# Kernel tuning notes

Hardware: AMD Instinct MI355X
Metric: run time of the kernel (lower is better)

The kernel has to match this reference:

```python
import jax, jax.numpy as jnp
import numpy as np

B, S, H = 4, 2048, 1024

def setup_inputs() -> dict:
    key = jax.random.key(0)
    k = jax.random.split(key, 5)
    scale = 1.0 / np.sqrt(H)
    return {
        "hidden": jax.random.normal(k[0], (B, S, H), dtype=jnp.float32),
        "mask": jnp.zeros((B, 1, S, S), dtype=jnp.float32),
        "R": jax.random.normal(k[1], (S, S), dtype=jnp.float32),
        "G_w": jax.random.normal(k[2], (H, H), dtype=jnp.float32) * scale,
        "G_b": jnp.zeros((H,), dtype=jnp.float32),
        "F_w": jax.random.normal(k[3], (H, H), dtype=jnp.float32) * scale,
        "F_b": jnp.zeros((H,), dtype=jnp.float32),
    }

def reference(hidden, mask, R, G_w, G_b, F_w, F_b):
    # scores: [B, S, S] = learned random bias + additive attention mask
    scores = R + mask[:, 0]
    probs = jax.nn.softmax(scores, axis=-1)  # dropout is identity in eval mode
    values = jnp.einsum('bsh,oh->bso', hidden, G_w) + G_b  # G_linear
    out = jnp.einsum('bqk,bkh->bqh', probs, values)
    out = jnp.einsum('bsh,oh->bso', out, F_w) + F_b  # final_linear
    return out
```

## Files before the change

### kernel.cpp

```cpp
#include <hip/hip_runtime.h>
#include <hip/hip_bf16.h>

typedef __bf16 bf16x8 __attribute__((ext_vector_type(8)));
typedef __bf16 bf16x4 __attribute__((ext_vector_type(4)));
typedef float  f32x16 __attribute__((ext_vector_type(16)));

#define GPTR(p) ((__attribute__((address_space(1))) void*)(p))
#define LPTR(p) ((__attribute__((address_space(3))) void*)(p))

__global__ __launch_bounds__(256) void pre_kernel(
    const float* __restrict__ Fw, __bf16* __restrict__ f_bf,
    const float* __restrict__ Gw, __bf16* __restrict__ gt_bf,
    const float* __restrict__ Gb, const float* __restrict__ Fb,
    float* __restrict__ b2, int H) {
    __shared__ float tile[64][65];
    const int blk = blockIdx.x;
    const int t = threadIdx.x;

    if (blk < 512) {
        long i = ((long)blk * 256 + t) * 8;
        float4 a = *reinterpret_cast<const float4*>(Fw + i);
        float4 c = *reinterpret_cast<const float4*>(Fw + i + 4);
        bf16x8 o;
        o[0] = (__bf16)a.x; o[1] = (__bf16)a.y; o[2] = (__bf16)a.z; o[3] = (__bf16)a.w;
        o[4] = (__bf16)c.x; o[5] = (__bf16)c.y; o[6] = (__bf16)c.z; o[7] = (__bf16)c.w;
        *reinterpret_cast<bf16x8*>(f_bf + i) = o;
    } else if (blk < 768) {
        const int id = blk - 512;
        const int bx = (id & 15) * 64;
        const int by = (id >> 4) * 64;
        const int tr = t >> 4;
        const int tc = (t & 15) * 4;
#pragma unroll
        for (int i = 0; i < 4; i++) {
            float4 v = *reinterpret_cast<const float4*>(&Gw[(size_t)(by + tr + i * 16) * H + bx + tc]);
            tile[tr + i * 16][tc + 0] = v.x;
            tile[tr + i * 16][tc + 1] = v.y;
            tile[tr + i * 16][tc + 2] = v.z;
            tile[tr + i * 16][tc + 3] = v.w;
        }
        __syncthreads();
        const int wr = t >> 2;
        const int wc = (t & 3) * 16;
        bf16x8 o0, o1;
#pragma unroll
        for (int j = 0; j < 8; j++) o0[j] = (__bf16)tile[wc + j][wr];
#pragma unroll
        for (int j = 0; j < 8; j++) o1[j] = (__bf16)tile[wc + 8 + j][wr];
        *reinterpret_cast<bf16x8*>(&gt_bf[(size_t)(bx + wr) * H + by + wc]) = o0;
        *reinterpret_cast<bf16x8*>(&gt_bf[(size_t)(bx + wr) * H + by + wc + 8]) = o1;
    } else {
        const int o = blk - 768;
        float s = 0.f;
        for (int h = t; h < H; h += 256) s += Fw[(size_t)o * H + h] * Gb[h];
#pragma unroll
        for (int off = 32; off > 0; off >>= 1) s += __shfl_xor(s, off);
        __shared__ float ss[4];
        if ((t & 63) == 0) ss[t >> 6] = s;
        __syncthreads();
        if (t == 0) b2[o] = ss[0] + ss[1] + ss[2] + ss[3] + Fb[o];
    }
}

__global__ __launch_bounds__(256) void mid_kernel(
    const __bf16* __restrict__ f_bf, const __bf16* __restrict__ gt_bf,
    __bf16* __restrict__ Wm,
    const float* __restrict__ hidden, __bf16* __restrict__ xt,
    const float* __restrict__ R, const float* __restrict__ mask,
    __bf16* __restrict__ P, int H, int S) {
    const int blk = blockIdx.x;
    const int t = threadIdx.x;

    if (blk < 256) {
        __shared__ __bf16 As[64 * 64];
        __shared__ __bf16 Bs[64 * 64];
        const int lane = t & 63;
        const int wave = t >> 6;
        const int lane31 = lane & 31;
        const int hi = lane >> 5;
        const int wm = (wave >> 1) * 32;
        const int wn = (wave & 1) * 32;
        const int bm = (blk >> 4) * 64;
        const int bn = (blk & 15) * 64;

        const int rsub = lane >> 3;
        const int csub = lane & 7;
        const int lchunk = csub ^ rsub;
        const __bf16* ga0 = f_bf + (size_t)(bm + wave * 16 + rsub) * H + lchunk * 8;
        const __bf16* gb0 = gt_bf + (size_t)(bn + wave * 16 + rsub) * H + lchunk * 8;

        f32x16 acc = (f32x16)(0.f);
        for (int kt = 0; kt < H; kt += 64) {
            __syncthreads();
#pragma unroll
            for (int c = 0; c < 2; c++)
                __builtin_amdgcn_global_load_lds(GPTR(ga0 + (size_t)(c * 8) * H + kt),
                                                 LPTR(&As[(wave * 16 + c * 8) * 64]), 16, 0, 0);
#pragma unroll
            for (int c = 0; c < 2; c++)
                __builtin_amdgcn_global_load_lds(GPTR(gb0 + (size_t)(c * 8) * H + kt),
                                                 LPTR(&Bs[(wave * 16 + c * 8) * 64]), 16, 0, 0);
            __syncthreads();
#pragma unroll
            for (int s = 0; s < 4; s++) {
                const int ra = wm + lane31;
                const int rb = wn + lane31;
                bf16x8 af = *reinterpret_cast<const bf16x8*>(
                    &As[ra * 64 + (((2 * s + hi) ^ (ra & 7)) << 3)]);
                bf16x8 bfr = *reinterpret_cast<const bf16x8*>(
                    &Bs[rb * 64 + (((2 * s + hi) ^ (rb & 7)) << 3)]);
                acc = __builtin_amdgcn_mfma_f32_32x32x16_bf16(af, bfr, acc, 0, 0, 0);
            }
        }
        const int cm = bm + wm;
        const int cn = bn + wn + lane31;
#pragma unroll
        for (int rq = 0; rq < 4; rq++) {
            const int rbase = rq * 8 + 4 * hi;
#pragma unroll
            for (int rr = 0; rr < 4; rr++)
                Wm[(size_t)(cm + rbase + rr) * H + cn] = (__bf16)acc[rq * 4 + rr];
        }
    } else if (blk < 2304) {
        __shared__ float tile[64][65];
        const int id = blk - 256;
        const int b = id >> 9;
        const int tid = id & 511;
        const int by = (tid >> 4) * 64;
        const int bx = (tid & 15) * 64;
        const float* x = hidden + (size_t)b * S * H;
        __bf16* y = xt + (size_t)b * H * S;
        const int tr = t >> 4;
        const int tc = (t & 15) * 4;
#pragma unroll
        for (int i = 0; i < 4; i++) {
            float4 v = *reinterpret_cast<const float4*>(&x[(size_t)(by + tr + i * 16) * H + bx + tc]);
            tile[tr + i * 16][tc + 0] = v.x;
            tile[tr + i * 16][tc + 1] = v.y;
            tile[tr + i * 16][tc + 2] = v.z;
            tile[tr + i * 16][tc + 3] = v.w;
        }
        __syncthreads();
        const int wr = t >> 2;
        const int wc = (t & 3) * 16;
        bf16x8 o0, o1;
#pragma unroll
        for (int j = 0; j < 8; j++) o0[j] = (__bf16)tile[wc + j][wr];
#pragma unroll
        for (int j = 0; j < 8; j++) o1[j] = (__bf16)tile[wc + 8 + j][wr];
        *reinterpret_cast<bf16x8*>(&y[(size_t)(bx + wr) * S + by + wc]) = o0;
        *reinterpret_cast<bf16x8*>(&y[(size_t)(bx + wr) * S + by + wc + 8]) = o1;
    } else {
        const int id = blk - 2304;
        const int b = id >> 11;
        const int q = id & 2047;
        const int lane = t & 63, wave = t >> 6;
        const float* rrow = R + (size_t)q * S;
        const float* mrow = mask + ((size_t)b * S + q) * (size_t)S;
        __bf16* prow = P + ((size_t)b * S + q) * (size_t)S;

        float v[8];
#pragma unroll
        for (int i = 0; i < 2; i++) {
            float4 r4 = *reinterpret_cast<const float4*>(rrow + t * 8 + i * 4);
            float4 m4 = *reinterpret_cast<const float4*>(mrow + t * 8 + i * 4);
            v[i * 4 + 0] = r4.x + m4.x;
            v[i * 4 + 1] = r4.y + m4.y;
            v[i * 4 + 2] = r4.z + m4.z;
            v[i * 4 + 3] = r4.w + m4.w;
        }
        float mx = v[0];
#pragma unroll
        for (int i = 1; i < 8; i++) mx = fmaxf(mx, v[i]);
#pragma unroll
        for (int off = 32; off > 0; off >>= 1) mx = fmaxf(mx, __shfl_xor(mx, off));
        __shared__ float smax[4], ssum[4];
        if (lane == 0) smax[wave] = mx;
        __syncthreads();
        mx = fmaxf(fmaxf(smax[0], smax[1]), fmaxf(smax[2], smax[3]));
        float sum = 0.f;
#pragma unroll
        for (int i = 0; i < 8; i++) { v[i] = __expf(v[i] - mx); sum += v[i]; }
#pragma unroll
        for (int off = 32; off > 0; off >>= 1) sum += __shfl_xor(sum, off);
        if (lane == 0) ssum[wave] = sum;
        __syncthreads();
        sum = ssum[0] + ssum[1] + ssum[2] + ssum[3];
        const float inv = 1.0f / sum;
        bf16x8 o;
#pragma unroll
        for (int i = 0; i < 8; i++) o[i] = (__bf16)(v[i] * inv);
        *reinterpret_cast<bf16x8*>(prow + t * 8) = o;
    }
}

template <bool CFLOAT, bool BIAS, int SWZMODE>
__global__ __launch_bounds__(256) void gemm_nt_kernel(
    const __bf16* __restrict__ A, const __bf16* __restrict__ B,
    const float* __restrict__ bias, void* __restrict__ Cv,
    int K, int lda, int ldb, int ldc,
    long strideA, long strideB, long strideC) {
    const int t = threadIdx.x;
    const int lane = t & 63;
    const int wave = t >> 6;
    const int lane31 = lane & 31;
    const int hi = lane >> 5;
    const int wm = (wave >> 1) * 64;
    const int wn = (wave & 1) * 64;
    int bm, bn, bz;
    if constexpr (SWZMODE == 1) {
        const int id = blockIdx.x;
        const int xcd = id & 7;
        const int slot = id >> 3;
        bz = xcd >> 1;
        bm = ((xcd & 1) * 8 + (slot >> 3)) * 128;
        bn = (slot & 7) * 128;
    } else {
        const int id = blockIdx.x;
        const int xcd = id & 7;
        const int slot = id >> 3;
        bz = 0;
        bm = (xcd * 8 + (slot >> 3)) * 128;
        bn = (slot & 7) * 128;
    }

    A += (size_t)bz * strideA;
    B += (size_t)bz * strideB;

    __shared__ __bf16 smem[32768];

    const int rsub = lane >> 3;
    const int csub = lane & 7;
    const int lchunk = csub ^ rsub;
    const __bf16* ga0 = A + (size_t)(bm + wave * 32 + rsub) * lda + lchunk * 8;
    const __bf16* gb0 = B + (size_t)(bn + wave * 32 + rsub) * ldb + lchunk * 8;

    auto stage = [&](int p, int kt) {
        __bf16* As_ = smem + p * 16384;
        __bf16* Bs_ = smem + p * 16384 + 8192;
#pragma unroll
        for (int c = 0; c < 4; c++)
            __builtin_amdgcn_global_load_lds(GPTR(ga0 + (size_t)(c * 8) * lda + kt),
                                             LPTR(&As_[(wave * 32 + c * 8) * 64]), 16, 0, 0);
#pragma unroll
        for (int c = 0; c < 4; c++)
            __builtin_amdgcn_global_load_lds(GPTR(gb0 + (size_t)(c * 8) * ldb + kt),
                                             LPTR(&Bs_[(wave * 32 + c * 8) * 64]), 16, 0, 0);
    };

    f32x16 acc[2][2];
#pragma unroll
    for (int i = 0; i < 2; i++)
#pragma unroll
        for (int j = 0; j < 2; j++) acc[i][j] = (f32x16)(0.f);

    stage(0, 0);
    __syncthreads();
    int p = 0;
    for (int kt = 0; kt < K; kt += 64) {
        if (kt + 64 < K) stage(p ^ 1, kt + 64);
        const __bf16* As = smem + p * 16384;
        const __bf16* Bs = smem + p * 16384 + 8192;
#pragma unroll
        for (int s = 0; s < 4; s++) {
            bf16x8 af[2], bfr[2];
#pragma unroll
            for (int mi = 0; mi < 2; mi++) {
                const int r = wm + mi * 32 + lane31;
                af[mi] = *reinterpret_cast<const bf16x8*>(
                    &As[r * 64 + (((2 * s + hi) ^ (r & 7)) << 3)]);
            }
#pragma unroll
            for (int ni = 0; ni < 2; ni++) {
                const int r = wn + ni * 32 + lane31;
                bfr[ni] = *reinterpret_cast<const bf16x8*>(
                    &Bs[r * 64 + (((2 * s + hi) ^ (r & 7)) << 3)]);
            }
#pragma unroll
            for (int mi = 0; mi < 2; mi++)
#pragma unroll
                for (int ni = 0; ni < 2; ni++)
                    acc[mi][ni] = __builtin_amdgcn_mfma_f32_32x32x16_bf16(af[mi], bfr[ni], acc[mi][ni], 0, 0, 0);
        }
        __syncthreads();
        p ^= 1;
    }

    __bf16* Cb = (__bf16*)Cv + (size_t)bz * strideC;
    float* Cf = (float*)Cv + (size_t)bz * strideC;
#pragma unroll
    for (int mi = 0; mi < 2; mi++)
#pragma unroll
        for (int ni = 0; ni < 2; ni++) {
            const int cm = bm + wm + mi * 32;
            const int cn = bn + wn + ni * 32 + lane31;
            const float bv = BIAS ? bias[cn] : 0.0f;
#pragma unroll
            for (int rq = 0; rq < 4; rq++) {
                const int rbase = rq * 8 + 4 * hi;
                if constexpr (CFLOAT) {
#pragma unroll
                    for (int rr = 0; rr < 4; rr++)
                        Cf[(size_t)(cm + rbase + rr) * ldc + cn] = acc[mi][ni][rq * 4 + rr] + bv;
                } else {
#pragma unroll
                    for (int rr = 0; rr < 4; rr++)
                        Cb[(size_t)(cm + rbase + rr) * ldc + cn] = (__bf16)(acc[mi][ni][rq * 4 + rr] + bv);
                }
            }
        }
}

extern "C" void kernel_launch(void* const* d_in, const int* in_sizes, int n_in,
                              void* d_out, int out_size, void* d_ws, size_t ws_size,
                              hipStream_t stream) {
    const float* hidden = (const float*)d_in[0];
    const float* mask   = (const float*)d_in[1];
    const float* R      = (const float*)d_in[2];
    const float* G_w    = (const float*)d_in[3];
    const float* G_b    = (const float*)d_in[4];
    const float* F_w    = (const float*)d_in[5];
    const float* F_b    = (const float*)d_in[6];
    float* out = (float*)d_out;

    constexpr int B = 4, S = 2048, H = 1024;
    char* ws = (char*)d_ws;
    __bf16* xt    = (__bf16*)(ws);
    __bf16* t1    = (__bf16*)(ws + (16ll << 20));
    __bf16* probs = (__bf16*)(ws + (32ll << 20));
    __bf16* f_bf  = (__bf16*)(ws + (64ll << 20));
    __bf16* gt_bf = (__bf16*)(ws + (66ll << 20));
    __bf16* Wm    = (__bf16*)(ws + (68ll << 20));
    float*  b2    = (float*)(ws + (70ll << 20));

    pre_kernel<<<1792, 256, 0, stream>>>(F_w, f_bf, G_w, gt_bf, G_b, F_b, b2, H);

    mid_kernel<<<10496, 256, 0, stream>>>(f_bf, gt_bf, Wm, hidden, xt,
                                          R, mask, probs, H, S);

    gemm_nt_kernel<false, false, 1><<<512, 256, 0, stream>>>(
        probs, xt, nullptr, t1, S, S, S, H,
        (long)S * S, (long)H * S, (long)S * H);

    gemm_nt_kernel<true, true, 2><<<512, 256, 0, stream>>>(
        t1, Wm, b2, out, H, H, H, H, 0, 0, 0);
}
```

Baseline: 222.7 us.

## Use 512-thread 256x128 GEMM with triple-buffered staged pipeline and wave-per-row softmax

Replaces the 128x128 double-buffered GEMM with a 512-thread, 256x128-tile kernel. It triple-buffers LDS, interleaves global-to-LDS prefetch between MFMA phases, and uses barriers, explicit waitcnt and setprio to overlap loads with compute. The softmax is changed to one wave per row so the block-level shared-memory reductions and syncthreads disappear. Mid-kernel shared memory is merged into a union to reduce its LDS footprint. The manual waitcnt and barrier scheduling is fragile and relies on the batch index being derived from bm, which only holds for the fixed shapes.

```diff
diff --git a/kernel.cpp b/kernel.cpp
--- a/kernel.cpp
+++ b/kernel.cpp
@@ -62,18 +62,24 @@
     }
 }
 
+union MidSmem {
+    struct { __bf16 a[64 * 64]; __bf16 b[64 * 64]; } g;
+    float tile[64][65];
+};
+
 __global__ __launch_bounds__(256) void mid_kernel(
     const __bf16* __restrict__ f_bf, const __bf16* __restrict__ gt_bf,
     __bf16* __restrict__ Wm,
     const float* __restrict__ hidden, __bf16* __restrict__ xt,
     const float* __restrict__ R, const float* __restrict__ mask,
     __bf16* __restrict__ P, int H, int S) {
+    __shared__ __align__(16) MidSmem sm;
     const int blk = blockIdx.x;
     const int t = threadIdx.x;
 
     if (blk < 256) {
-        __shared__ __bf16 As[64 * 64];
-        __shared__ __bf16 Bs[64 * 64];
+        __bf16* As = sm.g.a;
+        __bf16* Bs = sm.g.b;
         const int lane = t & 63;
         const int wave = t >> 6;
         const int lane31 = lane & 31;
@@ -122,7 +128,6 @@
                 Wm[(size_t)(cm + rbase + rr) * H + cn] = (__bf16)acc[rq * 4 + rr];
         }
     } else if (blk < 2304) {
-        __shared__ float tile[64][65];
         const int id = blk - 256;
         const int b = id >> 9;
         const int tid = id & 511;
@@ -135,35 +140,36 @@
 #pragma unroll
         for (int i = 0; i < 4; i++) {
             float4 v = *reinterpret_cast<const float4*>(&x[(size_t)(by + tr + i * 16) * H + bx + tc]);
-            tile[tr + i * 16][tc + 0] = v.x;
-            tile[tr + i * 16][tc + 1] = v.y;
-            tile[tr + i * 16][tc + 2] = v.z;
-            tile[tr + i * 16][tc + 3] = v.w;
+            sm.tile[tr + i * 16][tc + 0] = v.x;
+            sm.tile[tr + i * 16][tc + 1] = v.y;
+            sm.tile[tr + i * 16][tc + 2] = v.z;
+            sm.tile[tr + i * 16][tc + 3] = v.w;
         }
         __syncthreads();
         const int wr = t >> 2;
         const int wc = (t & 3) * 16;
         bf16x8 o0, o1;
 #pragma unroll
-        for (int j = 0; j < 8; j++) o0[j] = (__bf16)tile[wc + j][wr];
-#pragma unroll
-        for (int j = 0; j < 8; j++) o1[j] = (__bf16)tile[wc + 8 + j][wr];
+        for (int j = 0; j < 8; j++) o0[j] = (__bf16)sm.tile[wc + j][wr];
+#pragma unroll
+        for (int j = 0; j < 8; j++) o1[j] = (__bf16)sm.tile[wc + 8 + j][wr];
         *reinterpret_cast<bf16x8*>(&y[(size_t)(bx + wr) * S + by + wc]) = o0;
         *reinterpret_cast<bf16x8*>(&y[(size_t)(bx + wr) * S + by + wc + 8]) = o1;
     } else {
         const int id = blk - 2304;
-        const int b = id >> 11;
-        const int q = id & 2047;
         const int lane = t & 63, wave = t >> 6;
+        const int row = id * 4 + wave;
+        const int b = row >> 11;
+        const int q = row & 2047;
         const float* rrow = R + (size_t)q * S;
         const float* mrow = mask + ((size_t)b * S + q) * (size_t)S;
         __bf16* prow = P + ((size_t)b * S + q) * (size_t)S;
 
-        float v[8];
-#pragma unroll
-        for (int i = 0; i < 2; i++) {
-            float4 r4 = *reinterpret_cast<const float4*>(rrow + t * 8 + i * 4);
-            float4 m4 = *reinterpret_cast<const float4*>(mrow + t * 8 + i * 4);
+        float v[32];
+#pragma unroll
+        for (int i = 0; i < 8; i++) {
+            float4 r4 = *reinterpret_cast<const float4*>(rrow + i * 256 + lane * 4);
+            float4 m4 = *reinterpret_cast<const float4*>(mrow + i * 256 + lane * 4);
             v[i * 4 + 0] = r4.x + m4.x;
             v[i * 4 + 1] = r4.y + m4.y;
             v[i * 4 + 2] = r4.z + m4.z;
@@ -171,35 +177,30 @@
         }
         float mx = v[0];
 #pragma unroll
-        for (int i = 1; i < 8; i++) mx = fmaxf(mx, v[i]);
+        for (int i = 1; i < 32; i++) mx = fmaxf(mx, v[i]);
 #pragma unroll
         for (int off = 32; off > 0; off >>= 1) mx = fmaxf(mx, __shfl_xor(mx, off));
-        __shared__ float smax[4], ssum[4];
-        if (lane == 0) smax[wave] = mx;
-        __syncthreads();
-        mx = fmaxf(fmaxf(smax[0], smax[1]), fmaxf(smax[2], smax[3]));
         float sum = 0.f;
 #pragma unroll
-        for (int i = 0; i < 8; i++) { v[i] = __expf(v[i] - mx); sum += v[i]; }
+        for (int i = 0; i < 32; i++) { v[i] = __expf(v[i] - mx); sum += v[i]; }
 #pragma unroll
         for (int off = 32; off > 0; off >>= 1) sum += __shfl_xor(sum, off);
-        if (lane == 0) ssum[wave] = sum;
-        __syncthreads();
-        sum = ssum[0] + ssum[1] + ssum[2] + ssum[3];
         const float inv = 1.0f / sum;
-        bf16x8 o;
-#pragma unroll
-        for (int i = 0; i < 8; i++) o[i] = (__bf16)(v[i] * inv);
-        *reinterpret_cast<bf16x8*>(prow + t * 8) = o;
+#pragma unroll
+        for (int i = 0; i < 8; i++) {
+            bf16x4 o;
+#pragma unroll
+            for (int j = 0; j < 4; j++) o[j] = (__bf16)(v[i * 4 + j] * inv);
+            *reinterpret_cast<bf16x4*>(prow + i * 256 + lane * 4) = o;
+        }
     }
 }
 
-template <bool CFLOAT, bool BIAS, int SWZMODE>
-__global__ __launch_bounds__(256) void gemm_nt_kernel(
+template <bool CFLOAT, bool BIAS>
+__global__ __launch_bounds__(512, 2) void gemm8_nt(
     const __bf16* __restrict__ A, const __bf16* __restrict__ B,
     const float* __restrict__ bias, void* __restrict__ Cv,
-    int K, int lda, int ldb, int ldc,
-    long strideA, long strideB, long strideC) {
+    int K, int lda, int ldb, int ldc, long strideB) {
     const int t = threadIdx.x;
     const int lane = t & 63;
     const int wave = t >> 6;
@@ -207,46 +208,30 @@
     const int hi = lane >> 5;
     const int wm = (wave >> 1) * 64;
     const int wn = (wave & 1) * 64;
-    int bm, bn, bz;
-    if constexpr (SWZMODE == 1) {
-        const int id = blockIdx.x;
-        const int xcd = id & 7;
-        const int slot = id >> 3;
-        bz = xcd >> 1;
-        bm = ((xcd & 1) * 8 + (slot >> 3)) * 128;
-        bn = (slot & 7) * 128;
-    } else {
-        const int id = blockIdx.x;
-        const int xcd = id & 7;
-        const int slot = id >> 3;
-        bz = 0;
-        bm = (xcd * 8 + (slot >> 3)) * 128;
-        bn = (slot & 7) * 128;
-    }
-
-    A += (size_t)bz * strideA;
-    B += (size_t)bz * strideB;
-
-    __shared__ __bf16 smem[32768];
+
+    const int id = blockIdx.x;
+    const int xcd = id & 7;
+    const int slot = id >> 3;
+    const int bm = (xcd * 4 + (slot >> 3)) * 256;
+    const int bn = (slot & 7) * 128;
+    B += (size_t)(bm >> 11) * strideB;
+
+    __shared__ __align__(16) __bf16 smem[3 * 24576];
 
     const int rsub = lane >> 3;
     const int csub = lane & 7;
     const int lchunk = csub ^ rsub;
     const __bf16* ga0 = A + (size_t)(bm + wave * 32 + rsub) * lda + lchunk * 8;
-    const __bf16* gb0 = B + (size_t)(bn + wave * 32 + rsub) * ldb + lchunk * 8;
-
-    auto stage = [&](int p, int kt) {
-        __bf16* As_ = smem + p * 16384;
-        __bf16* Bs_ = smem + p * 16384 + 8192;
-#pragma unroll
-        for (int c = 0; c < 4; c++)
-            __builtin_amdgcn_global_load_lds(GPTR(ga0 + (size_t)(c * 8) * lda + kt),
-                                             LPTR(&As_[(wave * 32 + c * 8) * 64]), 16, 0, 0);
-#pragma unroll
-        for (int c = 0; c < 4; c++)
-            __builtin_amdgcn_global_load_lds(GPTR(gb0 + (size_t)(c * 8) * ldb + kt),
-                                             LPTR(&Bs_[(wave * 32 + c * 8) * 64]), 16, 0, 0);
+    const __bf16* gb0 = B + (size_t)(bn + wave * 16 + rsub) * ldb + lchunk * 8;
+
+    auto stageA = [&](int p, int kt, int c) {
+        __builtin_amdgcn_global_load_lds(GPTR(ga0 + (size_t)(c * 8) * lda + kt),
+                                         LPTR(&smem[p * 24576 + (wave * 32 + c * 8) * 64]), 16, 0, 0);
     };
+    auto stageBv = [&](int p, int kt, int c) {
+        __builtin_amdgcn_global_load_lds(GPTR(gb0 + (size_t)(c * 8) * ldb + kt),
+                                         LPTR(&smem[p * 24576 + 16384 + (wave * 16 + c * 8) * 64]), 16, 0, 0);
+    };
 
     f32x16 acc[2][2];
 #pragma unroll
@@ -254,40 +239,89 @@
 #pragma unroll
         for (int j = 0; j < 2; j++) acc[i][j] = (f32x16)(0.f);
 
-    stage(0, 0);
-    __syncthreads();
-    int p = 0;
-    for (int kt = 0; kt < K; kt += 64) {
-        if (kt + 64 < K) stage(p ^ 1, kt + 64);
-        const __bf16* As = smem + p * 16384;
-        const __bf16* Bs = smem + p * 16384 + 8192;
+    const int nt = K >> 6;
+#pragma unroll
+    for (int c = 0; c < 4; c++) stageA(0, 0, c);
+#pragma unroll
+    for (int c = 0; c < 2; c++) stageBv(0, 0, c);
+#pragma unroll
+    for (int c = 0; c < 4; c++) stageA(1, 64, c);
+#pragma unroll
+    for (int c = 0; c < 2; c++) stageBv(1, 64, c);
+    asm volatile("s_waitcnt vmcnt(6)" ::: "memory");
+    __builtin_amdgcn_s_barrier();
+
+    const int ra0 = wm + lane31;
+    const int ra1 = wm + 32 + lane31;
+    const int rb0 = wn + lane31;
+    const int rb1 = wn + 32 + lane31;
+    const int ca = lane31 & 7;
+
+    int cur = 0;
+    for (int it = 0; it < nt; ++it) {
+        const __bf16* As = smem + cur * 24576;
+        const __bf16* Bs = smem + cur * 24576 + 16384;
+        const int kt2 = (it + 2) << 6;
+        const bool pre = (it + 2) < nt;
+        const int p2 = (cur >= 1) ? cur - 1 : 2;
+        bf16x8 a0[4], a1[4], b0[4], b1[4];
+
 #pragma unroll
         for (int s = 0; s < 4; s++) {
-            bf16x8 af[2], bfr[2];
-#pragma unroll
-            for (int mi = 0; mi < 2; mi++) {
-                const int r = wm + mi * 32 + lane31;
-                af[mi] = *reinterpret_cast<const bf16x8*>(
-                    &As[r * 64 + (((2 * s + hi) ^ (r & 7)) << 3)]);
-            }
-#pragma unroll
-            for (int ni = 0; ni < 2; ni++) {
-                const int r = wn + ni * 32 + lane31;
-                bfr[ni] = *reinterpret_cast<const bf16x8*>(
-                    &Bs[r * 64 + (((2 * s + hi) ^ (r & 7)) << 3)]);
-            }
-#pragma unroll
-            for (int mi = 0; mi < 2; mi++)
-#pragma unroll
-                for (int ni = 0; ni < 2; ni++)
-                    acc[mi][ni] = __builtin_amdgcn_mfma_f32_32x32x16_bf16(af[mi], bfr[ni], acc[mi][ni], 0, 0, 0);
-        }
-        __syncthreads();
-        p ^= 1;
+            a0[s] = *reinterpret_cast<const bf16x8*>(&As[ra0 * 64 + (((2 * s + hi) ^ ca) << 3)]);
+            b0[s] = *reinterpret_cast<const bf16x8*>(&Bs[rb0 * 64 + (((2 * s + hi) ^ ca) << 3)]);
+        }
+        __builtin_amdgcn_s_barrier();
+        asm volatile("s_waitcnt lgkmcnt(0)");
+        __builtin_amdgcn_s_setprio(1);
+#pragma unroll
+        for (int s = 0; s < 4; s++)
+            acc[0][0] = __builtin_amdgcn_mfma_f32_32x32x16_bf16(a0[s], b0[s], acc[0][0], 0, 0, 0);
+        __builtin_amdgcn_s_setprio(0);
+        __builtin_amdgcn_s_barrier();
+
+#pragma unroll
+        for (int s = 0; s < 4; s++)
+            b1[s] = *reinterpret_cast<const bf16x8*>(&Bs[rb1 * 64 + (((2 * s + hi) ^ ca) << 3)]);
+        if (pre) { stageA(p2, kt2, 0); stageA(p2, kt2, 1); }
+        __builtin_amdgcn_s_barrier();
+        asm volatile("s_waitcnt lgkmcnt(0)");
+        __builtin_amdgcn_s_setprio(1);
+#pragma unroll
+        for (int s = 0; s < 4; s++)
+            acc[0][1] = __builtin_amdgcn_mfma_f32_32x32x16_bf16(a0[s], b1[s], acc[0][1], 0, 0, 0);
+        __builtin_amdgcn_s_setprio(0);
+        __builtin_amdgcn_s_barrier();
+
+#pragma unroll
+        for (int s = 0; s < 4; s++)
+            a1[s] = *reinterpret_cast<const bf16x8*>(&As[ra1 * 64 + (((2 * s + hi) ^ ca) << 3)]);
+        if (pre) { stageA(p2, kt2, 2); stageA(p2, kt2, 3); }
+        __builtin_amdgcn_s_barrier();
+        asm volatile("s_waitcnt lgkmcnt(0)");
+        __builtin_amdgcn_s_setprio(1);
+#pragma unroll
+        for (int s = 0; s < 4; s++)
+            acc[1][1] = __builtin_amdgcn_mfma_f32_32x32x16_bf16(a1[s], b1[s], acc[1][1], 0, 0, 0);
+        __builtin_amdgcn_s_setprio(0);
+        __builtin_amdgcn_s_barrier();
+
+        if (pre) { stageBv(p2, kt2, 0); stageBv(p2, kt2, 1); }
+        if (it + 1 < nt) {
+            if (pre) asm volatile("s_waitcnt vmcnt(6)" ::: "memory");
+            else     asm volatile("s_waitcnt vmcnt(0)" ::: "memory");
+        }
+        __builtin_amdgcn_s_barrier();
+        __builtin_amdgcn_s_setprio(1);
+#pragma unroll
+        for (int s = 0; s < 4; s++)
+            acc[1][0] = __builtin_amdgcn_mfma_f32_32x32x16_bf16(a1[s], b0[s], acc[1][0], 0, 0, 0);
+        __builtin_amdgcn_s_setprio(0);
+        cur = (cur == 2) ? 0 : cur + 1;
     }
 
-    __bf16* Cb = (__bf16*)Cv + (size_t)bz * strideC;
-    float* Cf = (float*)Cv + (size_t)bz * strideC;
+    __bf16* Cb = (__bf16*)Cv;
+    float* Cf = (float*)Cv;
 #pragma unroll
     for (int mi = 0; mi < 2; mi++)
 #pragma unroll
@@ -335,13 +369,12 @@
 
     pre_kernel<<<1792, 256, 0, stream>>>(F_w, f_bf, G_w, gt_bf, G_b, F_b, b2, H);
 
-    mid_kernel<<<10496, 256, 0, stream>>>(f_bf, gt_bf, Wm, hidden, xt,
-                                          R, mask, probs, H, S);
-
-    gemm_nt_kernel<false, false, 1><<<512, 256, 0, stream>>>(
-        probs, xt, nullptr, t1, S, S, S, H,
-        (long)S * S, (long)H * S, (long)S * H);
-
-    gemm_nt_kernel<true, true, 2><<<512, 256, 0, stream>>>(
-        t1, Wm, b2, out, H, H, H, H, 0, 0, 0);
+    mid_kernel<<<4352, 256, 0, stream>>>(f_bf, gt_bf, Wm, hidden, xt,
+                                         R, mask, probs, H, S);
+
+    gemm8_nt<false, false><<<256, 512, 0, stream>>>(
+        probs, xt, nullptr, t1, S, S, S, H, (long)H * S);
+
+    gemm8_nt<true, true><<<256, 512, 0, stream>>>(
+        t1, Wm, b2, out, H, H, H, H, 0);
 }
```

New measurement: 227.8 us. 1.02x slower.

## Reassociate to project hidden first and fuse fp32-to-bf16 conversion into GEMM

Applied to the files above, without the earlier changes.

Reorders the matmul chain so hidden is multiplied by the fused weight matrix first, producing a transposed bf16 intermediate, and then the probability matrix multiplies that result with bias in the epilogue. The new GEMM reads fp32 hidden directly and converts to bf16 while staging into shared memory, removing the separate transpose/convert pass and the t1 intermediate. This trades a dedicated transpose kernel for register-staged B loads and strided transposed output stores, which may be less efficient.

```diff
diff --git a/kernel.cpp b/kernel.cpp
--- a/kernel.cpp
+++ b/kernel.cpp
@@ -62,18 +62,23 @@
     }
 }
 
+union MidSmem {
+    struct { __bf16 a[64 * 64]; __bf16 b[64 * 64]; } g;
+    float red[8];
+};
+
 __global__ __launch_bounds__(256) void mid_kernel(
     const __bf16* __restrict__ f_bf, const __bf16* __restrict__ gt_bf,
     __bf16* __restrict__ Wm,
-    const float* __restrict__ hidden, __bf16* __restrict__ xt,
     const float* __restrict__ R, const float* __restrict__ mask,
     __bf16* __restrict__ P, int H, int S) {
+    __shared__ __align__(16) MidSmem sm;
     const int blk = blockIdx.x;
     const int t = threadIdx.x;
 
     if (blk < 256) {
-        __shared__ __bf16 As[64 * 64];
-        __shared__ __bf16 Bs[64 * 64];
+        __bf16* As = sm.g.a;
+        __bf16* Bs = sm.g.b;
         const int lane = t & 63;
         const int wave = t >> 6;
         const int lane31 = lane & 31;
@@ -121,37 +126,8 @@
             for (int rr = 0; rr < 4; rr++)
                 Wm[(size_t)(cm + rbase + rr) * H + cn] = (__bf16)acc[rq * 4 + rr];
         }
-    } else if (blk < 2304) {
-        __shared__ float tile[64][65];
+    } else {
         const int id = blk - 256;
-        const int b = id >> 9;
-        const int tid = id & 511;
-        const int by = (tid >> 4) * 64;
-        const int bx = (tid & 15) * 64;
-        const float* x = hidden + (size_t)b * S * H;
-        __bf16* y = xt + (size_t)b * H * S;
-        const int tr = t >> 4;
-        const int tc = (t & 15) * 4;
-#pragma unroll
-        for (int i = 0; i < 4; i++) {
-            float4 v = *reinterpret_cast<const float4*>(&x[(size_t)(by + tr + i * 16) * H + bx + tc]);
-            tile[tr + i * 16][tc + 0] = v.x;
-            tile[tr + i * 16][tc + 1] = v.y;
-            tile[tr + i * 16][tc + 2] = v.z;
-            tile[tr + i * 16][tc + 3] = v.w;
-        }
-        __syncthreads();
-        const int wr = t >> 2;
-        const int wc = (t & 3) * 16;
-        bf16x8 o0, o1;
-#pragma unroll
-        for (int j = 0; j < 8; j++) o0[j] = (__bf16)tile[wc + j][wr];
-#pragma unroll
-        for (int j = 0; j < 8; j++) o1[j] = (__bf16)tile[wc + 8 + j][wr];
-        *reinterpret_cast<bf16x8*>(&y[(size_t)(bx + wr) * S + by + wc]) = o0;
-        *reinterpret_cast<bf16x8*>(&y[(size_t)(bx + wr) * S + by + wc + 8]) = o1;
-    } else {
-        const int id = blk - 2304;
         const int b = id >> 11;
         const int q = id & 2047;
         const int lane = t & 63, wave = t >> 6;
@@ -174,18 +150,17 @@
         for (int i = 1; i < 8; i++) mx = fmaxf(mx, v[i]);
 #pragma unroll
         for (int off = 32; off > 0; off >>= 1) mx = fmaxf(mx, __shfl_xor(mx, off));
-        __shared__ float smax[4], ssum[4];
-        if (lane == 0) smax[wave] = mx;
-        __syncthreads();
-        mx = fmaxf(fmaxf(smax[0], smax[1]), fmaxf(smax[2], smax[3]));
+        if (lane == 0) sm.red[wave] = mx;
+        __syncthreads();
+        mx = fmaxf(fmaxf(sm.red[0], sm.red[1]), fmaxf(sm.red[2], sm.red[3]));
         float sum = 0.f;
 #pragma unroll
         for (int i = 0; i < 8; i++) { v[i] = __expf(v[i] - mx); sum += v[i]; }
 #pragma unroll
         for (int off = 32; off > 0; off >>= 1) sum += __shfl_xor(sum, off);
-        if (lane == 0) ssum[wave] = sum;
-        __syncthreads();
-        sum = ssum[0] + ssum[1] + ssum[2] + ssum[3];
+        if (lane == 0) sm.red[4 + wave] = sum;
+        __syncthreads();
+        sum = sm.red[4] + sm.red[5] + sm.red[6] + sm.red[7];
         const float inv = 1.0f / sum;
         bf16x8 o;
 #pragma unroll
@@ -194,7 +169,120 @@
     }
 }
 
-template <bool CFLOAT, bool BIAS, int SWZMODE>
+__global__ __launch_bounds__(256) void gemm_wy_kernel(
+    const __bf16* __restrict__ Wm, const float* __restrict__ hidden,
+    __bf16* __restrict__ Yt) {
+    constexpr int H = 1024, S = 2048, K = 1024;
+    const int t = threadIdx.x;
+    const int lane = t & 63;
+    const int wave = t >> 6;
+    const int lane31 = lane & 31;
+    const int hi = lane >> 5;
+    const int wm = (wave >> 1) * 64;
+    const int wn = (wave & 1) * 64;
+    const int id = blockIdx.x;
+    const int xcd = id & 7;
+    const int slot = id >> 3;
+    const int bm = (slot & 7) * 128;
+    const int bn = (xcd * 8 + (slot >> 3)) * 128;
+
+    __shared__ __align__(16) __bf16 smem[32768];
+
+    const int rsub = lane >> 3;
+    const int csub = lane & 7;
+    const int lchunk = csub ^ rsub;
+    const __bf16* ga0 = Wm + (size_t)(bm + wave * 32 + rsub) * K + lchunk * 8;
+
+    auto stageA = [&](int p, int kt) {
+#pragma unroll
+        for (int c = 0; c < 4; c++)
+            __builtin_amdgcn_global_load_lds(GPTR(ga0 + (size_t)(c * 8) * K + kt),
+                LPTR(&smem[p * 16384 + (wave * 32 + c * 8) * 64]), 16, 0, 0);
+    };
+
+    const int q4 = t & 15;
+    const int rr = t >> 4;
+    const int cg = q4 >> 1;
+    const int h8 = (q4 & 1) * 4;
+    float4 br[8];
+    auto loadB = [&](int kt) {
+#pragma unroll
+        for (int i = 0; i < 8; i++)
+            br[i] = *reinterpret_cast<const float4*>(
+                hidden + (size_t)(bn + rr + i * 16) * K + kt + q4 * 4);
+    };
+    auto writeB = [&](int p) {
+#pragma unroll
+        for (int i = 0; i < 8; i++) {
+            const int r = rr + i * 16;
+            bf16x4 o;
+            o[0] = (__bf16)br[i].x; o[1] = (__bf16)br[i].y;
+            o[2] = (__bf16)br[i].z; o[3] = (__bf16)br[i].w;
+            *reinterpret_cast<bf16x4*>(
+                &smem[p * 16384 + 8192 + r * 64 + ((cg ^ (r & 7)) << 3) + h8]) = o;
+        }
+    };
+
+    f32x16 acc[2][2];
+#pragma unroll
+    for (int i = 0; i < 2; i++)
+#pragma unroll
+        for (int j = 0; j < 2; j++) acc[i][j] = (f32x16)(0.f);
+
+    loadB(0);
+    stageA(0, 0);
+    writeB(0);
+    __syncthreads();
+    int p = 0;
+    for (int kt = 0; kt < K; kt += 64) {
+        const bool pre = kt + 64 < K;
+        if (pre) { loadB(kt + 64); stageA(p ^ 1, kt + 64); }
+        const __bf16* As = smem + p * 16384;
+        const __bf16* Bs = smem + p * 16384 + 8192;
+#pragma unroll
+        for (int s = 0; s < 4; s++) {
+            bf16x8 af[2], bfr[2];
+#pragma unroll
+            for (int mi = 0; mi < 2; mi++) {
+                const int r = wm + mi * 32 + lane31;
+                af[mi] = *reinterpret_cast<const bf16x8*>(
+                    &As[r * 64 + (((2 * s + hi) ^ (r & 7)) << 3)]);
+            }
+#pragma unroll
+            for (int ni = 0; ni < 2; ni++) {
+                const int r = wn + ni * 32 + lane31;
+                bfr[ni] = *reinterpret_cast<const bf16x8*>(
+                    &Bs[r * 64 + (((2 * s + hi) ^ (r & 7)) << 3)]);
+            }
+#pragma unroll
+            for (int mi = 0; mi < 2; mi++)
+#pragma unroll
+                for (int ni = 0; ni < 2; ni++)
+                    acc[mi][ni] = __builtin_amdgcn_mfma_f32_32x32x16_bf16(af[mi], bfr[ni], acc[mi][ni], 0, 0, 0);
+        }
+        if (pre) writeB(p ^ 1);
+        __syncthreads();
+        p ^= 1;
+    }
+
+#pragma unroll
+    for (int mi = 0; mi < 2; mi++)
+#pragma unroll
+        for (int ni = 0; ni < 2; ni++) {
+            const int cm = bm + wm + mi * 32;
+            const int cnf = bn + wn + ni * 32 + lane31;
+            __bf16* Cb = Yt + (size_t)(cnf >> 11) * H * S + (cnf & 2047);
+#pragma unroll
+            for (int rq = 0; rq < 4; rq++) {
+                const int rbase = rq * 8 + 4 * hi;
+#pragma unroll
+                for (int rrq = 0; rrq < 4; rrq++)
+                    Cb[(size_t)(cm + rbase + rrq) * S] = (__bf16)acc[mi][ni][rq * 4 + rrq];
+            }
+        }
+}
+
+template <bool CFLOAT, bool BIAS>
 __global__ __launch_bounds__(256) void gemm_nt_kernel(
     const __bf16* __restrict__ A, const __bf16* __restrict__ B,
     const float* __restrict__ bias, void* __restrict__ Cv,
@@ -207,27 +295,17 @@
     const int hi = lane >> 5;
     const int wm = (wave >> 1) * 64;
     const int wn = (wave & 1) * 64;
-    int bm, bn, bz;
-    if constexpr (SWZMODE == 1) {
-        const int id = blockIdx.x;
-        const int xcd = id & 7;
-        const int slot = id >> 3;
-        bz = xcd >> 1;
-        bm = ((xcd & 1) * 8 + (slot >> 3)) * 128;
-        bn = (slot & 7) * 128;
-    } else {
-        const int id = blockIdx.x;
-        const int xcd = id & 7;
-        const int slot = id >> 3;
-        bz = 0;
-        bm = (xcd * 8 + (slot >> 3)) * 128;
-        bn = (slot & 7) * 128;
-    }
+    const int id = blockIdx.x;
+    const int xcd = id & 7;
+    const int slot = id >> 3;
+    const int bz = xcd >> 1;
+    const int bm = ((xcd & 1) * 8 + (slot >> 3)) * 128;
+    const int bn = (slot & 7) * 128;
 
     A += (size_t)bz * strideA;
     B += (size_t)bz * strideB;
 
-    __shared__ __bf16 smem[32768];
+    __shared__ __align__(16) __bf16 smem[32768];
 
     const int rsub = lane >> 3;
     const int csub = lane & 7;
@@ -325,23 +403,20 @@
 
     constexpr int B = 4, S = 2048, H = 1024;
     char* ws = (char*)d_ws;
-    __bf16* xt    = (__bf16*)(ws);
-    __bf16* t1    = (__bf16*)(ws + (16ll << 20));
-    __bf16* probs = (__bf16*)(ws + (32ll << 20));
-    __bf16* f_bf  = (__bf16*)(ws + (64ll << 20));
-    __bf16* gt_bf = (__bf16*)(ws + (66ll << 20));
-    __bf16* Wm    = (__bf16*)(ws + (68ll << 20));
-    float*  b2    = (float*)(ws + (70ll << 20));
+    __bf16* probs = (__bf16*)(ws);
+    __bf16* yt    = (__bf16*)(ws + (32ll << 20));
+    __bf16* f_bf  = (__bf16*)(ws + (48ll << 20));
+    __bf16* gt_bf = (__bf16*)(ws + (50ll << 20));
+    __bf16* Wm    = (__bf16*)(ws + (52ll << 20));
+    float*  b2    = (float*)(ws + (54ll << 20));
 
     pre_kernel<<<1792, 256, 0, stream>>>(F_w, f_bf, G_w, gt_bf, G_b, F_b, b2, H);
 
-    mid_kernel<<<10496, 256, 0, stream>>>(f_bf, gt_bf, Wm, hidden, xt,
-                                          R, mask, probs, H, S);
-
-    gemm_nt_kernel<false, false, 1><<<512, 256, 0, stream>>>(
-        probs, xt, nullptr, t1, S, S, S, H,
+    mid_kernel<<<8448, 256, 0, stream>>>(f_bf, gt_bf, Wm, R, mask, probs, H, S);
+
+    gemm_wy_kernel<<<512, 256, 0, stream>>>(Wm, hidden, yt);
+
+    gemm_nt_kernel<true, true><<<512, 256, 0, stream>>>(
+        probs, yt, b2, out, S, S, S, H,
         (long)S * S, (long)H * S, (long)S * H);
-
-    gemm_nt_kernel<true, true, 2><<<512, 256, 0, stream>>>(
-        t1, Wm, b2, out, H, H, H, H, 0, 0, 0);
 }
```

New measurement: 229.4 us. 3.0% more time.
